# Optimization experiments

Hardware: AMD Instinct MI355X
Metric: run time of the kernel (lower is better)

The kernel has to match this reference:

```python
import jax, jax.numpy as jnp
import numpy as np

B, N, DIM = 4, 2048, 1024
HEADS, DIM_HEAD = 16, 64
HIDDEN = HEADS * DIM_HEAD  # 1024
SCALE = 1.0 / np.sqrt(DIM_HEAD).astype(np.float32)


def setup_inputs() -> dict:
    key = jax.random.key(0)
    k1, k2, k3 = jax.random.split(key, 3)
    x = jax.random.normal(k1, (B, N, DIM), dtype=jnp.float32)
    # Linear(dim, 3*hidden, bias=False): stored as [in, out] for x @ W
    w_qkv = jax.random.normal(k2, (DIM, 3 * HIDDEN), dtype=jnp.float32) * (1.0 / np.sqrt(DIM))
    w_out = jax.random.normal(k3, (HIDDEN, DIM), dtype=jnp.float32) * (1.0 / np.sqrt(HIDDEN))
    b_out = jnp.zeros((DIM,), dtype=jnp.float32)
    return {"x": x, "w_qkv": w_qkv, "w_out": w_out, "b_out": b_out}


def reference(x, w_qkv, w_out, b_out):
    b, n, _ = x.shape
    qkv = x @ w_qkv                                  # [b, n, 3*hidden]
    q, k, v = jnp.split(qkv, 3, axis=-1)             # each [b, n, hidden]

    def to_heads(t):
        return t.reshape(b, n, HEADS, DIM_HEAD).transpose(0, 2, 1, 3)  # [b, h, n, d]

    q, k, v = to_heads(q), to_heads(k), to_heads(v)
    scores = jnp.einsum('bhid,bhjd->bhij', q, k) * SCALE   # [b, h, n_q, n_k]
    # Faithful to original: softmax over dim=2 (the QUERY axis), not keys.
    attn = jax.nn.softmax(scores, axis=2)
    y = jnp.einsum('bhij,bhjd->bhid', attn, v)             # [b, h, n, d]
    y = y.transpose(0, 2, 1, 3).reshape(b, n, HIDDEN)      # [b, n, hidden]
    return y @ w_out + b_out
```

## Files before the change

kernel.cpp:

```cpp
#include <hip/hip_runtime.h>
#include <math.h>
#include <stdint.h>

#define B_    4
#define N_    2048
#define DIM_  1024
#define H_    16
#define DH_   64
#define HID_  1024
#define RS_   3072
#define C2_   0.1803368801111204f

typedef unsigned short u16;
typedef unsigned int   u32;
typedef short  bf16x8 __attribute__((ext_vector_type(8)));
typedef u16    u16x8  __attribute__((ext_vector_type(8)));
typedef float  f32x4  __attribute__((ext_vector_type(4)));
typedef float  f32x16 __attribute__((ext_vector_type(16)));
typedef unsigned int u32x2 __attribute__((ext_vector_type(2)));

__device__ inline u16 f2b(float x) {
    u32 u = __float_as_uint(x);
    return (u16)((u + 0x7fffu + ((u >> 16) & 1u)) >> 16);
}
__device__ inline float b2f(u16 x) {
    return __uint_as_float((u32)x << 16);
}

__device__ inline u32 pack2bf(float f0, float f1) {
    u32 u0 = __float_as_uint(f0) + 0x8000u;
    u32 u1 = __float_as_uint(f1) + 0x8000u;
    return __builtin_amdgcn_perm(u1, u0, 0x07060302u);
}

__device__ inline void pl32swap(u32 &a, u32 &b) {
#if __has_builtin(__builtin_amdgcn_permlane32_swap)
    u32x2 r = __builtin_amdgcn_permlane32_swap(a, b, false, false);
    a = r[0]; b = r[1];
#else
    asm("v_permlane32_swap_b32 %0, %1" : "+v"(a), "+v"(b));
#endif
}

#if defined(__has_builtin)
#if __has_builtin(__builtin_amdgcn_global_load_lds)
#define USE_GLL 1
#endif
#endif

#ifdef USE_GLL
typedef const __attribute__((address_space(1))) u32* gas_ptr;
typedef __attribute__((address_space(3))) u32* las_ptr;
__device__ inline void gll16(const void* g, void* l) {
    __builtin_amdgcn_global_load_lds((gas_ptr)g, (las_ptr)l, 16, 0, 0);
}
#endif

__global__ __launch_bounds__(256) void cast_bf16(const float* __restrict__ in,
                                                 u16* __restrict__ out, int n) {
    int i = (blockIdx.x * 256 + threadIdx.x) * 8;
    if (i >= n) return;
    float4 a = *(const float4*)&in[i];
    float4 b = *(const float4*)&in[i + 4];
    u16x8 p;
    p[0] = f2b(a.x); p[1] = f2b(a.y); p[2] = f2b(a.z); p[3] = f2b(a.w);
    p[4] = f2b(b.x); p[5] = f2b(b.y); p[6] = f2b(b.z); p[7] = f2b(b.w);
    *(u16x8*)&out[i] = p;
}

__global__ __launch_bounds__(256) void transpose_cast(const float* __restrict__ W,
                                                      u16* __restrict__ Wt,
                                                      int K, int Nn, int qcols) {
    __shared__ float t[64][65];
    const int tid = threadIdx.x;
    const int k0 = blockIdx.y * 64, n0 = blockIdx.x * 64;
    for (int idx = tid; idx < 64 * 16; idx += 256) {
        int r = idx >> 4, c4 = (idx & 15) * 4;
        float4 g = *(const float4*)&W[(size_t)(k0 + r) * Nn + n0 + c4];
        t[r][c4] = g.x; t[r][c4 + 1] = g.y; t[r][c4 + 2] = g.z; t[r][c4 + 3] = g.w;
    }
    __syncthreads();
    for (int idx = tid; idx < 64 * 8; idx += 256) {
        int n = idx >> 3, k8 = (idx & 7) * 8;
        float s = (n0 + n < qcols) ? C2_ : 1.0f;
        u16x8 p;
        #pragma unroll
        for (int u = 0; u < 8; u++) p[u] = f2b(t[k8 + u][n] * s);
        *(u16x8*)&Wt[(size_t)(n0 + n) * K + k0 + k8] = p;
    }
}

template<int BF16OUT>
__global__ __launch_bounds__(256) void gemm_bt(const u16* __restrict__ A,
                                               const u16* __restrict__ Bt,
                                               const float* __restrict__ bias,
                                               void* __restrict__ Cout,
                                               int M, int Nn, int K) {
    __shared__ u16 at[128 * 64];
    __shared__ u16 bt[128 * 64];
    const int tid = threadIdx.x;
    const int lane = tid & 63, wave = tid >> 6;
    const int wr = wave >> 1, wc = wave & 1;
    const int mlane = lane & 15, quad = lane >> 4;
    const int id = blockIdx.x;
    const int mt = (id & 7) * 8 + ((id >> 3) & 7);
    const int nt = id >> 6;
    const int m0 = mt * 128, n0 = nt * 128;
    const int r = tid >> 3, kc = (tid & 7) * 8;
    const int kcs = kc ^ ((r & 7) * 8);

    f32x4 acc[4][4] = {};

    for (int k0 = 0; k0 < K; k0 += 64) {
        __syncthreads();
#ifdef USE_GLL
        #pragma unroll
        for (int i = 0; i < 4; i++) {
            gll16(&A [(size_t)(m0 + r + 32 * i) * K + k0 + kcs], &at[(r + 32 * i) * 64 + kc]);
            gll16(&Bt[(size_t)(n0 + r + 32 * i) * K + k0 + kcs], &bt[(r + 32 * i) * 64 + kc]);
        }
#else
        #pragma unroll
        for (int i = 0; i < 4; i++) {
            *(u16x8*)&at[(r + 32 * i) * 64 + kc] = *(const u16x8*)&A [(size_t)(m0 + r + 32 * i) * K + k0 + kcs];
            *(u16x8*)&bt[(r + 32 * i) * 64 + kc] = *(const u16x8*)&Bt[(size_t)(n0 + r + 32 * i) * K + k0 + kcs];
        }
#endif
        __syncthreads();

        #pragma unroll
        for (int ks = 0; ks < 2; ks++) {
            bf16x8 af[4], bf[4];
            #pragma unroll
            for (int rt = 0; rt < 4; rt++) {
                int row = wr * 64 + rt * 16 + mlane;
                af[rt] = *(const bf16x8*)&at[row * 64 + ((ks * 32 + quad * 8) ^ ((row & 7) * 8))];
            }
            #pragma unroll
            for (int ct = 0; ct < 4; ct++) {
                int row = wc * 64 + ct * 16 + mlane;
                bf[ct] = *(const bf16x8*)&bt[row * 64 + ((ks * 32 + quad * 8) ^ ((row & 7) * 8))];
            }
            #pragma unroll
            for (int rt = 0; rt < 4; rt++)
                #pragma unroll
                for (int ct = 0; ct < 4; ct++)
                    acc[rt][ct] = __builtin_amdgcn_mfma_f32_16x16x32_bf16(af[rt], bf[ct], acc[rt][ct], 0, 0, 0);
        }
    }

    const int row0 = m0 + wr * 64 + quad * 4;
    const int col0 = n0 + wc * 64 + mlane;
    #pragma unroll
    for (int rt = 0; rt < 4; rt++)
        #pragma unroll
        for (int ct = 0; ct < 4; ct++) {
            int c = col0 + ct * 16;
            float bv = (!BF16OUT && bias != nullptr) ? bias[c] : 0.f;
            #pragma unroll
            for (int reg = 0; reg < 4; reg++) {
                int rr = row0 + rt * 16 + reg;
                float v = acc[rt][ct][reg] + bv;
                if (BF16OUT) ((u16*)Cout)[(size_t)rr * Nn + c] = f2b(v);
                else         ((float*)Cout)[(size_t)rr * Nn + c] = v;
            }
        }
}

__global__ __launch_bounds__(256) void attn_stats_vt(const u16* __restrict__ qkvb,
                                                     u16* __restrict__ vT) {
    __shared__ u16 kt[64 * 72];
    __shared__ u16 qt[4][64 * 72];
    __shared__ float red[4][64];
    __shared__ float li[64];

    const int tid = threadIdx.x;
    const int lane = tid & 63, wave = tid >> 6;
    const int mlane = lane & 15, quad = lane >> 4;
    const int id = blockIdx.x;
    const int bh = (id & 7) * 8 + ((id >> 3) & 7);
    const int b = bh >> 4, h = bh & 15;
    const int j0 = (id >> 6) * 64;

    const u16* qbase = qkvb + (size_t)b * N_ * RS_ + h * DH_;
    const u16* kbase = qbase + HID_;
    const u16* vbase = qbase + 2 * HID_;

    for (int idx = tid; idx < 512; idx += 256) {
        int r = idx >> 3, d8 = (idx & 7) * 8;
        *(u16x8*)&kt[r * 72 + d8] = *(const u16x8*)&kbase[(size_t)(j0 + r) * RS_ + d8];
    }
    __syncthreads();

    bf16x8 kf[4][2];
    #pragma unroll
    for (int t = 0; t < 4; t++)
        #pragma unroll
        for (int ks = 0; ks < 2; ks++)
            kf[t][ks] = *(const bf16x8*)&kt[(t * 16 + mlane) * 72 + ks * 32 + quad * 8];

    f32x4 acc[4] = {};
    u16* qw = &qt[wave][0];

    const int prr = lane >> 3, pd8 = (lane & 7) * 8;
    u16x8 pq[8];
    #pragma unroll
    for (int t = 0; t < 8; t++)
        pq[t] = *(const u16x8*)&qbase[(size_t)(wave * 64 + t * 8 + prr) * RS_ + pd8];

    for (int i0 = wave * 64; i0 < N_; i0 += 256) {
        #pragma unroll
        for (int t = 0; t < 8; t++)
            *(u16x8*)&qw[(t * 8 + prr) * 72 + pd8] = pq[t];
        int in = i0 + 256;
        if (in < N_) {
            #pragma unroll
            for (int t = 0; t < 8; t++)
                pq[t] = *(const u16x8*)&qbase[(size_t)(in + t * 8 + prr) * RS_ + pd8];
        }
        #pragma unroll
        for (int q4 = 0; q4 < 4; q4++) {
            bf16x8 bq0 = *(const bf16x8*)&qw[(q4 * 16 + mlane) * 72 + quad * 8];
            bf16x8 bq1 = *(const bf16x8*)&qw[(q4 * 16 + mlane) * 72 + 32 + quad * 8];
            #pragma unroll
            for (int t = 0; t < 4; t++) {
                f32x4 z = {0.f, 0.f, 0.f, 0.f};
                z = __builtin_amdgcn_mfma_f32_16x16x32_bf16(kf[t][0], bq0, z, 0, 0, 0);
                z = __builtin_amdgcn_mfma_f32_16x16x32_bf16(kf[t][1], bq1, z, 0, 0, 0);
                #pragma unroll
                for (int reg = 0; reg < 4; reg++)
                    acc[t][reg] += __builtin_amdgcn_exp2f(z[reg]);
            }
        }
    }

    #pragma unroll
    for (int t = 0; t < 4; t++)
        #pragma unroll
        for (int reg = 0; reg < 4; reg++) {
            float v = acc[t][reg];
            v += __shfl_xor(v, 1, 64);
            v += __shfl_xor(v, 2, 64);
            v += __shfl_xor(v, 4, 64);
            v += __shfl_xor(v, 8, 64);
            if (mlane == 0) red[wave][t * 16 + quad * 4 + reg] = v;
        }
    __syncthreads();
    if (tid < 64) {
        float l = red[0][tid] + red[1][tid] + red[2][tid] + red[3][tid];
        li[tid] = 1.0f / l;
    }

    for (int idx = tid; idx < 512; idx += 256) {
        int r = idx >> 3, d8 = (idx & 7) * 8;
        *(u16x8*)&kt[r * 72 + d8] = *(const u16x8*)&vbase[(size_t)(j0 + r) * RS_ + d8];
    }
    __syncthreads();
    {
        int d = tid >> 2, j16 = (tid & 3) * 16;
        u16x8 p0, p1;
        #pragma unroll
        for (int u = 0; u < 8; u++) {
            p0[u] = f2b(b2f(kt[(j16 + u) * 72 + d]) * li[j16 + u]);
            p1[u] = f2b(b2f(kt[(j16 + 8 + u) * 72 + d]) * li[j16 + 8 + u]);
        }
        size_t o = ((size_t)bh * DH_ + d) * N_ + j0 + j16;
        *(u16x8*)&vT[o] = p0;
        *(u16x8*)&vT[o + 8] = p1;
    }
}

__global__ __launch_bounds__(512) void attn_apply(const u16* __restrict__ qkvb,
                                                  const u16* __restrict__ vT,
                                                  u16* __restrict__ yb) {
    __shared__ u16 S[256 * 72];

    const int tid = threadIdx.x;
    const int lane = tid & 63, wave = tid >> 6;
    const int m31 = lane & 31, half = lane >> 5;

    const int id = blockIdx.x;
    const int v = (id & 7) * 64 + (id >> 3);
    const int bh = v >> 3, b = bh >> 4, h = bh & 15;
    const int i0 = (v & 7) * 256;

    const u16* qbase = qkvb + (size_t)b * N_ * RS_ + h * DH_;
    const u16* kbase = qbase + HID_;
    const u16* vbase = vT + (size_t)bh * DH_ * N_;

    for (int idx = tid; idx < 2048; idx += 512) {
        int r = idx >> 3, d8 = (idx & 7) * 8;
        *(u16x8*)&S[r * 72 + d8] = *(const u16x8*)&qbase[(size_t)(i0 + r) * RS_ + d8];
    }
    __syncthreads();

    bf16x8 qf[4];
    #pragma unroll
    for (int ks = 0; ks < 4; ks++)
        qf[ks] = *(const bf16x8*)&S[(wave * 32 + m31) * 72 + ks * 16 + half * 8];

    const int pr = tid >> 3, pc8 = (tid & 7) * 8;
    u16x8 pk, pv;
    pk = *(const u16x8*)&kbase[(size_t)pr * RS_ + pc8];
    pv = *(const u16x8*)&vbase[(size_t)pr * N_ + pc8];

    __syncthreads();

    f32x16 yacc[2] = {};

    int cur = 0;
    for (int j0 = 0; j0 < N_; j0 += 64, cur ^= 1) {
        u16* Sb = &S[cur * 128 * 72];
        *(u16x8*)&Sb[pr * 72 + pc8]        = pk;
        *(u16x8*)&Sb[(pr + 64) * 72 + pc8] = pv;
        __syncthreads();

        int jn = j0 + 64;
        if (jn < N_) {
            pk = *(const u16x8*)&kbase[(size_t)(jn + pr) * RS_ + pc8];
            pv = *(const u16x8*)&vbase[(size_t)pr * N_ + jn + pc8];
        }

        bf16x8 pa[4];
        #pragma unroll
        for (int kt = 0; kt < 2; kt++) {
            bf16x8 ka[4];
            #pragma unroll
            for (int ks = 0; ks < 4; ks++)
                ka[ks] = *(const bf16x8*)&Sb[(kt * 32 + m31) * 72 + ks * 16 + half * 8];

            f32x16 sc = {};
            __builtin_amdgcn_s_setprio(1);
            #pragma unroll
            for (int ks = 0; ks < 4; ks++)
                sc = __builtin_amdgcn_mfma_f32_32x32x16_bf16(ka[ks], qf[ks], sc, 0, 0, 0);
            __builtin_amdgcn_s_setprio(0);

            u32 P[4][2];
            #pragma unroll
            for (int rb = 0; rb < 4; rb++)
                #pragma unroll
                for (int pp = 0; pp < 2; pp++) {
                    float e0 = __builtin_amdgcn_exp2f(sc[4 * rb + 2 * pp]);
                    float e1 = __builtin_amdgcn_exp2f(sc[4 * rb + 2 * pp + 1]);
                    P[rb][pp] = pack2bf(e0, e1);
                }
            #pragma unroll
            for (int ksl = 0; ksl < 2; ksl++) {
                pl32swap(P[2 * ksl][0], P[2 * ksl + 1][0]);
                pl32swap(P[2 * ksl][1], P[2 * ksl + 1][1]);
                union { u32 u[4]; bf16x8 v; } cv;
                cv.u[0] = P[2 * ksl][0];
                cv.u[1] = P[2 * ksl][1];
                cv.u[2] = P[2 * ksl + 1][0];
                cv.u[3] = P[2 * ksl + 1][1];
                pa[2 * kt + ksl] = cv.v;
            }
        }

        __builtin_amdgcn_s_setprio(1);
        #pragma unroll
        for (int ks16 = 0; ks16 < 4; ks16++) {
            bf16x8 vb0 = *(const bf16x8*)&Sb[(64 + m31) * 72 + ks16 * 16 + half * 8];
            bf16x8 vb1 = *(const bf16x8*)&Sb[(96 + m31) * 72 + ks16 * 16 + half * 8];
            yacc[0] = __builtin_amdgcn_mfma_f32_32x32x16_bf16(pa[ks16], vb0, yacc[0], 0, 0, 0);
            yacc[1] = __builtin_amdgcn_mfma_f32_32x32x16_bf16(pa[ks16], vb1, yacc[1], 0, 0, 0);
        }
        __builtin_amdgcn_s_setprio(0);
    }

    #pragma unroll
    for (int dt = 0; dt < 2; dt++)
        #pragma unroll
        for (int reg = 0; reg < 16; reg++) {
            int q = i0 + wave * 32 + (reg & 3) + 8 * (reg >> 2) + 4 * half;
            yb[((size_t)b * N_ + q) * HID_ + h * DH_ + dt * 32 + m31] = f2b(yacc[dt][reg]);
        }
}

extern "C" void kernel_launch(void* const* d_in, const int* in_sizes, int n_in,
                              void* d_out, int out_size, void* d_ws, size_t ws_size,
                              hipStream_t stream) {
    (void)in_sizes; (void)n_in; (void)out_size; (void)ws_size;

    const float* x     = (const float*)d_in[0];
    const float* w_qkv = (const float*)d_in[1];
    const float* w_out = (const float*)d_in[2];
    const float* b_out = (const float*)d_in[3];

    u16* xb    = (u16*)d_ws;
    u16* wqkvT = xb    + (size_t)8192 * 1024;
    u16* woutT = wqkvT + (size_t)3072 * 1024;
    u16* qkvb  = woutT + (size_t)1024 * 1024;
    u16* vTb   = qkvb  + (size_t)8192 * 3072;
    u16* yb    = vTb   + (size_t)64 * 64 * 2048;

    cast_bf16<<<4096, 256, 0, stream>>>(x, xb, 8192 * 1024);
    transpose_cast<<<dim3(3072 / 64, 1024 / 64), 256, 0, stream>>>(w_qkv, wqkvT, 1024, 3072, HID_);
    transpose_cast<<<dim3(1024 / 64, 1024 / 64), 256, 0, stream>>>(w_out, woutT, 1024, 1024, 0);

    gemm_bt<1><<<64 * 24, 256, 0, stream>>>(
        xb, wqkvT, nullptr, qkvb, 8192, 3072, 1024);

    attn_stats_vt<<<32 * 64, 256, 0, stream>>>(qkvb, vTb);

    attn_apply<<<512, 512, 0, stream>>>(qkvb, vTb, yb);

    gemm_bt<0><<<64 * 8, 256, 0, stream>>>(
        yb, woutT, b_out, d_out, 8192, 1024, 1024);
}
```

Measured before the change: 329.1 us.

## Add 256x256 double-buffered 8-wave GEMM for QKV projection

Adds a new bf16 GEMM kernel for the QKV projection. It uses 256x256 output tiles across 512 threads, double-buffers its LDS staging with global_load_lds, and interleaves each quarter-tile load with MFMA phases under explicit vmcnt waits, barriers and setprio. The goal is to hide global-load latency behind compute and raise data reuse per tile compared with the single-buffered 128x128 kernel. In exchange it needs 128KB of LDS per block, which limits occupancy, and it relies on a hand-scheduled barrier sequence that could stall if the phase ordering is off.

```diff
diff --git a/kernel.cpp b/kernel.cpp
--- a/kernel.cpp
+++ b/kernel.cpp
@@ -42,19 +42,15 @@
 #endif
 }
 
-#if defined(__has_builtin)
-#if __has_builtin(__builtin_amdgcn_global_load_lds)
-#define USE_GLL 1
-#endif
-#endif
-
-#ifdef USE_GLL
 typedef const __attribute__((address_space(1))) u32* gas_ptr;
 typedef __attribute__((address_space(3))) u32* las_ptr;
 __device__ inline void gll16(const void* g, void* l) {
+#if defined(__HIP_DEVICE_COMPILE__) && __has_builtin(__builtin_amdgcn_global_load_lds)
     __builtin_amdgcn_global_load_lds((gas_ptr)g, (las_ptr)l, 16, 0, 0);
-}
+#else
+    *(u16x8*)l = *(const u16x8*)g;
 #endif
+}
 
 __global__ __launch_bounds__(256) void cast_bf16(const float* __restrict__ in,
                                                  u16* __restrict__ out, int n) {
@@ -113,19 +109,11 @@
 
     for (int k0 = 0; k0 < K; k0 += 64) {
         __syncthreads();
-#ifdef USE_GLL
         #pragma unroll
         for (int i = 0; i < 4; i++) {
             gll16(&A [(size_t)(m0 + r + 32 * i) * K + k0 + kcs], &at[(r + 32 * i) * 64 + kc]);
             gll16(&Bt[(size_t)(n0 + r + 32 * i) * K + k0 + kcs], &bt[(r + 32 * i) * 64 + kc]);
         }
-#else
-        #pragma unroll
-        for (int i = 0; i < 4; i++) {
-            *(u16x8*)&at[(r + 32 * i) * 64 + kc] = *(const u16x8*)&A [(size_t)(m0 + r + 32 * i) * K + k0 + kcs];
-            *(u16x8*)&bt[(r + 32 * i) * 64 + kc] = *(const u16x8*)&Bt[(size_t)(n0 + r + 32 * i) * K + k0 + kcs];
-        }
-#endif
         __syncthreads();
 
         #pragma unroll
@@ -165,6 +153,149 @@
                 else         ((float*)Cout)[(size_t)rr * Nn + c] = v;
             }
         }
+}
+
+#define STAGE_A8(buf_, h_, k0_) do { \
+    const u16* s_ = &A[(size_t)(m0 + (h_) * 128 + sr) * K + (k0_) + kcs]; \
+    gll16(s_, &at[buf_][h_][sr * 64 + kc]); \
+    gll16(s_ + (size_t)64 * K, &at[buf_][h_][(sr + 64) * 64 + kc]); \
+} while (0)
+
+#define STAGE_B8(buf_, h_, k0_) do { \
+    const u16* s_ = &Bt[(size_t)(n0 + (h_) * 128 + sr) * K + (k0_) + kcs]; \
+    gll16(s_, &bt[buf_][h_][sr * 64 + kc]); \
+    gll16(s_ + (size_t)64 * K, &bt[buf_][h_][(sr + 64) * 64 + kc]); \
+} while (0)
+
+#define READ_AF8(b_, h_) do { \
+    _Pragma("unroll") \
+    for (int mf = 0; mf < 4; ++mf) { \
+        int row_ = wm * 64 + mf * 16 + mlane; int sw_ = (row_ & 7) * 8; \
+        af[mf][0] = *(const bf16x8*)&at[b_][h_][row_ * 64 + ((quad * 8) ^ sw_)]; \
+        af[mf][1] = *(const bf16x8*)&at[b_][h_][row_ * 64 + ((32 + quad * 8) ^ sw_)]; \
+    } \
+} while (0)
+
+#define READ_BF8(dst_, b_, h_) do { \
+    _Pragma("unroll") \
+    for (int nf = 0; nf < 2; ++nf) { \
+        int row_ = wn4 * 32 + nf * 16 + mlane; int sw_ = (row_ & 7) * 8; \
+        dst_[nf][0] = *(const bf16x8*)&bt[b_][h_][row_ * 64 + ((quad * 8) ^ sw_)]; \
+        dst_[nf][1] = *(const bf16x8*)&bt[b_][h_][row_ * 64 + ((32 + quad * 8) ^ sw_)]; \
+    } \
+} while (0)
+
+#define MFMA_PHASE8(p_, BF_) do { \
+    __builtin_amdgcn_s_setprio(1); \
+    _Pragma("unroll") \
+    for (int mf = 0; mf < 4; ++mf) \
+        _Pragma("unroll") \
+        for (int nf = 0; nf < 2; ++nf) { \
+            acc[p_][mf][nf] = __builtin_amdgcn_mfma_f32_16x16x32_bf16(af[mf][0], BF_[nf][0], acc[p_][mf][nf], 0, 0, 0); \
+            acc[p_][mf][nf] = __builtin_amdgcn_mfma_f32_16x16x32_bf16(af[mf][1], BF_[nf][1], acc[p_][mf][nf], 0, 0, 0); \
+        } \
+    __builtin_amdgcn_s_setprio(0); \
+} while (0)
+
+#define VMWAIT8(n_) do { \
+    asm volatile("s_waitcnt vmcnt(" #n_ ")" ::: "memory"); \
+    __builtin_amdgcn_sched_barrier(0); \
+} while (0)
+
+__global__ __launch_bounds__(512, 2) void gemm_bt8(const u16* __restrict__ A,
+                                                   const u16* __restrict__ Bt,
+                                                   u16* __restrict__ Cout,
+                                                   int M, int Nn, int K) {
+    __shared__ u16 at[2][2][128 * 64];
+    __shared__ u16 bt[2][2][128 * 64];
+    const int tid = threadIdx.x;
+    const int lane = tid & 63, wave = tid >> 6;
+    const int wm = wave >> 2, wn4 = wave & 3;
+    const int mlane = lane & 15, quad = lane >> 4;
+    const int ntx = Nn >> 8;
+    const int nblk = (M >> 8) * ntx;
+    const int id = blockIdx.x;
+    const int v = (id & 7) * (nblk >> 3) + (id >> 3);
+    const int mt = v / ntx, nt = v - mt * ntx;
+    const int m0 = mt * 256, n0 = nt * 256;
+    const int sr = tid >> 3, kc = (tid & 7) * 8;
+    const int kcs = kc ^ ((sr & 7) * 8);
+
+    f32x4 acc[4][4][2] = {};
+    bf16x8 af[4][2], bf0[2][2], bf1[2][2];
+
+    const int NT = K >> 6;
+
+    STAGE_A8(0, 0, 0); STAGE_B8(0, 0, 0); STAGE_B8(0, 1, 0); STAGE_A8(0, 1, 0);
+    VMWAIT8(4);
+    __builtin_amdgcn_s_barrier();
+
+    for (int t = 0; t < NT - 1; ++t) {
+        const int b = t & 1, nb = b ^ 1;
+        const int kn = (t + 1) << 6;
+
+        READ_AF8(b, 0);
+        READ_BF8(bf0, b, 0);
+        STAGE_A8(nb, 0, kn);
+        __builtin_amdgcn_s_barrier();
+        MFMA_PHASE8(0, bf0);
+        VMWAIT8(4);
+        __builtin_amdgcn_s_barrier();
+
+        READ_BF8(bf1, b, 1);
+        STAGE_B8(nb, 0, kn);
+        __builtin_amdgcn_s_barrier();
+        MFMA_PHASE8(1, bf1);
+        VMWAIT8(4);
+        __builtin_amdgcn_s_barrier();
+
+        READ_AF8(b, 1);
+        STAGE_B8(nb, 1, kn);
+        __builtin_amdgcn_s_barrier();
+        MFMA_PHASE8(2, bf0);
+        __builtin_amdgcn_s_barrier();
+
+        STAGE_A8(nb, 1, kn);
+        __builtin_amdgcn_s_barrier();
+        MFMA_PHASE8(3, bf1);
+        VMWAIT8(4);
+        __builtin_amdgcn_s_barrier();
+    }
+
+    {
+        const int b = (NT - 1) & 1;
+        READ_AF8(b, 0);
+        READ_BF8(bf0, b, 0);
+        __builtin_amdgcn_s_barrier();
+        MFMA_PHASE8(0, bf0);
+        VMWAIT8(2);
+        __builtin_amdgcn_s_barrier();
+
+        READ_BF8(bf1, b, 1);
+        __builtin_amdgcn_s_barrier();
+        MFMA_PHASE8(1, bf1);
+        VMWAIT8(0);
+        __builtin_amdgcn_s_barrier();
+
+        READ_AF8(b, 1);
+        __builtin_amdgcn_s_barrier();
+        MFMA_PHASE8(2, bf0);
+        __builtin_amdgcn_s_barrier();
+        MFMA_PHASE8(3, bf1);
+    }
+
+    #pragma unroll
+    for (int p = 0; p < 4; ++p) {
+        const int rbase = m0 + (p >> 1) * 128 + wm * 64 + quad * 4;
+        const int cbase = n0 + (p & 1) * 128 + wn4 * 32 + mlane;
+        #pragma unroll
+        for (int mf = 0; mf < 4; ++mf)
+            #pragma unroll
+            for (int nf = 0; nf < 2; ++nf)
+                #pragma unroll
+                for (int reg = 0; reg < 4; ++reg)
+                    Cout[(size_t)(rbase + mf * 16 + reg) * Nn + cbase + nf * 16] = f2b(acc[p][mf][nf][reg]);
+    }
 }
 
 __global__ __launch_bounds__(256) void attn_stats_vt(const u16* __restrict__ qkvb,
@@ -399,8 +530,7 @@
     transpose_cast<<<dim3(3072 / 64, 1024 / 64), 256, 0, stream>>>(w_qkv, wqkvT, 1024, 3072, HID_);
     transpose_cast<<<dim3(1024 / 64, 1024 / 64), 256, 0, stream>>>(w_out, woutT, 1024, 1024, 0);
 
-    gemm_bt<1><<<64 * 24, 256, 0, stream>>>(
-        xb, wqkvT, nullptr, qkvb, 8192, 3072, 1024);
+    gemm_bt8<<<384, 512, 0, stream>>>(xb, wqkvT, qkvb, 8192, 3072, 1024);
 
     attn_stats_vt<<<32 * 64, 256, 0, stream>>>(qkvb, vTb);
 
```

After: 321.4 us. 2.3% less time.
